# Kernel optimization log

Measured on AMD Instinct MI355X. Metric: run time of the kernel, lower is better.

Reference implementation:

```python
import jax, jax.numpy as jnp
import numpy as np

# dims
P = 512          # perception_vector_size
A_DIM = 64       # action_vector_size
D_MODEL = 256
D_STATE = 16
D_CONV = 4
D_INNER = 2 * D_MODEL      # expand=2 -> 512
DT_RANK = D_MODEL // 16    # ceil(256/16) = 16
BATCH = 8192


def setup_inputs() -> dict:
    key = jax.random.key(0)
    ks = jax.random.split(key, 12)
    s = lambda k, shp, sc=0.02: (jax.random.normal(k, shp, jnp.float32) * sc)
    return {
        "perception": jax.random.normal(ks[0], (BATCH, P), jnp.float32),
        # Brain linears
        "W_in": s(ks[1], (D_MODEL, P)), "b_in": jnp.zeros((D_MODEL,), jnp.float32),
        "mu_w": s(ks[2], (A_DIM, D_MODEL)), "mu_b": jnp.zeros((A_DIM,), jnp.float32),
        "ls_w": s(ks[3], (A_DIM, D_MODEL)), "ls_b": jnp.zeros((A_DIM,), jnp.float32),
        # Mamba params (mamba_ssm Mamba(d_model=256, d_state=16, d_conv=4, expand=2))
        "in_proj_w": s(ks[4], (2 * D_INNER, D_MODEL)),            # no bias
        "conv_w": s(ks[5], (D_INNER, D_CONV), 0.1),               # depthwise causal conv
        "conv_b": jnp.zeros((D_INNER,), jnp.float32),
        "x_proj_w": s(ks[6], (DT_RANK + 2 * D_STATE, D_INNER)),   # no bias
        "dt_proj_w": s(ks[7], (D_INNER, DT_RANK), 0.1),
        "dt_proj_b": s(ks[8], (D_INNER,), 0.1),
        # S4D real init: A_log[d, n] = log(n+1)
        "A_log": jnp.log(jnp.broadcast_to(jnp.arange(1, D_STATE + 1, dtype=jnp.float32), (D_INNER, D_STATE))),
        "Dskip": jnp.ones((D_INNER,), jnp.float32),
        "out_proj_w": s(ks[9], (D_MODEL, D_INNER)),               # no bias
    }


def _mamba(x, in_proj_w, conv_w, conv_b, x_proj_w, dt_proj_w, dt_proj_b, A_log, Dskip):
    # x: [B, L, d_model]
    Bsz, L, _ = x.shape
    xz = x @ in_proj_w.T                       # [B, L, 2*D_INNER]
    u, z = jnp.split(xz, 2, axis=-1)           # each [B, L, D_INNER]
    # causal depthwise conv1d (padding d_conv-1 on the left), then SiLU
    u_pad = jnp.pad(u, ((0, 0), (D_CONV - 1, 0), (0, 0)))
    idx = jnp.arange(L)[:, None] + jnp.arange(D_CONV)[None, :]   # [L, K]
    windows = u_pad[:, idx, :]                 # [B, L, K, D_INNER]
    u = jnp.einsum('blkc,ck->blc', windows, conv_w) + conv_b
    u = jax.nn.silu(u)
    # input-dependent SSM params
    x_dbl = u @ x_proj_w.T                     # [B, L, dt_rank + 2*d_state]
    dt, Bm, Cm = jnp.split(x_dbl, [DT_RANK, DT_RANK + D_STATE], axis=-1)
    delta = jax.nn.softplus(dt @ dt_proj_w.T + dt_proj_b)  # [B, L, D_INNER]
    A = -jnp.exp(A_log)                        # [D_INNER, D_STATE]

    def step(h, inp):
        u_t, dl, b_t, c_t = inp                # [B,D],[B,D],[B,N],[B,N]
        dA = jnp.exp(dl[..., None] * A)        # [B, D, N]
        h = dA * h + dl[..., None] * b_t[:, None, :] * u_t[..., None]
        y = jnp.einsum('bdn,bn->bd', h, c_t)
        return h, y

    h0 = jnp.zeros((Bsz, D_INNER, D_STATE), u.dtype)
    xs = (u.transpose(1, 0, 2), delta.transpose(1, 0, 2),
          Bm.transpose(1, 0, 2), Cm.transpose(1, 0, 2))
    _, ys = jax.lax.scan(step, h0, xs)         # ys: [L, B, D_INNER]
    y = ys.transpose(1, 0, 2) + Dskip * u      # skip connection D*u
    return y * jax.nn.silu(z)


def reference(perception, W_in, b_in, mu_w, mu_b, ls_w, ls_b,
              in_proj_w, conv_w, conv_b, x_proj_w, dt_proj_w, dt_proj_b,
              A_log, Dskip, out_proj_w):
    x = (perception @ W_in.T + b_in)[:, None, :]     # [B, 1, d_model]
    y = _mamba(x, in_proj_w, conv_w, conv_b, x_proj_w,
               dt_proj_w, dt_proj_b, A_log, Dskip)   # [B, 1, D_INNER]
    h = (y @ out_proj_w.T)[:, 0, :]                  # [B, d_model]
    mu = jnp.tanh(h @ mu_w.T + mu_b)
    log_std = jnp.clip(h @ ls_w.T + ls_b, -5.0, 2.0)
    return mu, log_std
```

## Files before the change

kernel.cpp:

```cpp
#include <hip/hip_runtime.h>
#include <hip/hip_fp16.h>
#include <cmath>

#define BATCH 8192

typedef short bf16x8 __attribute__((ext_vector_type(8)));
typedef float f32x4 __attribute__((ext_vector_type(4)));
typedef float f32x16 __attribute__((ext_vector_type(16)));

__device__ __forceinline__ void split2(float x, unsigned short& h, unsigned short& l){
    unsigned u = __float_as_uint(x);
    unsigned hr = u + 0x7fffu + ((u >> 16) & 1u);
    unsigned short hs = (unsigned short)(hr >> 16);
    float hf = __uint_as_float(((unsigned)hs) << 16);
    float d = x - hf;
    unsigned v = __float_as_uint(d);
    unsigned short ls = (unsigned short)((v + 0x7fffu + ((v >> 16) & 1u)) >> 16);
    h = hs; l = ls;
}
__device__ __forceinline__ float fsig(float x){ return 1.f / (1.f + __expf(-x)); }
__device__ __forceinline__ float ftanh(float x){
    x = fminf(fmaxf(x, -10.f), 10.f);
    const float e = __expf(2.f*x);
    return (e - 1.f) / (e + 1.f);
}
__device__ __forceinline__ void async_copy16(void* lds, const void* g){
    __builtin_amdgcn_global_load_lds(
        (const __attribute__((address_space(1))) unsigned int*)g,
        (__attribute__((address_space(3))) unsigned int*)lds, 16, 0, 0);
}


__global__ __launch_bounds__(256) void prep_all(
    const float* __restrict__ percep,
    const float* __restrict__ in_proj, const float* __restrict__ W_in,
    const float* __restrict__ b_in,
    const float* __restrict__ mu_w, const float* __restrict__ ls_w,
    const float* __restrict__ conv_w, const float* __restrict__ conv_b,
    const float* __restrict__ out_proj, const float* __restrict__ x_proj,
    unsigned short* __restrict__ W1h, unsigned short* __restrict__ W1l,
    unsigned short* __restrict__ Wth, unsigned short* __restrict__ Wtl,
    unsigned short* __restrict__ Xph, unsigned short* __restrict__ Xpl,
    unsigned short* __restrict__ Ph, unsigned short* __restrict__ Pl,
    float* __restrict__ b1)
{
    __shared__ float As[16][68];
    __shared__ float Ws[16][68];
    __shared__ unsigned short Lh[4096];
    __shared__ unsigned short Ll[4096];

    const int bx = blockIdx.x, by = blockIdx.y;
    const int tid = threadIdx.x;
    if (bx >= 20){
        const int s = (bx-20)*8 + by;
        const int band = s >> 4, ks = s & 15;
        const size_t tbase = (size_t)s*4096;
#pragma unroll
        for (int g=0; g<2; ++g){
            const int u = g*256 + tid;
            const int row = u >> 2, piece = u & 3;
            const float* src = percep + (size_t)(band*128 + row)*512 + ks*32 + piece*8;
            const float4 v0 = *reinterpret_cast<const float4*>(src);
            const float4 v1 = *reinterpret_cast<const float4*>(src+4);
            unsigned short h[8], l[8];
            split2(v0.x,h[0],l[0]); split2(v0.y,h[1],l[1]);
            split2(v0.z,h[2],l[2]); split2(v0.w,h[3],l[3]);
            split2(v1.x,h[4],l[4]); split2(v1.y,h[5],l[5]);
            split2(v1.z,h[6],l[6]); split2(v1.w,h[7],l[7]);
            uint4 H, L;
            H.x=(unsigned)h[0]|((unsigned)h[1]<<16); H.y=(unsigned)h[2]|((unsigned)h[3]<<16);
            H.z=(unsigned)h[4]|((unsigned)h[5]<<16); H.w=(unsigned)h[6]|((unsigned)h[7]<<16);
            L.x=(unsigned)l[0]|((unsigned)l[1]<<16); L.y=(unsigned)l[2]|((unsigned)l[3]<<16);
            L.z=(unsigned)l[4]|((unsigned)l[5]<<16); L.w=(unsigned)l[6]|((unsigned)l[7]<<16);
            const int off = piece*1024 + row*8;
            *reinterpret_cast<uint4*>(&Lh[off]) = H;
            *reinterpret_cast<uint4*>(&Ll[off]) = L;
        }
        __syncthreads();
#pragma unroll
        for (int g=0; g<2; ++g){
            const int f = g*256 + tid;
            *reinterpret_cast<uint4*>(&Ph[tbase + f*8]) = *reinterpret_cast<const uint4*>(&Lh[f*8]);
            *reinterpret_cast<uint4*>(&Pl[tbase + f*8]) = *reinterpret_cast<const uint4*>(&Ll[f*8]);
        }
        return;
    }
    if (bx == 18){
        const int lane = tid & 63, w = tid >> 6;
        const float4 bv = *reinterpret_cast<const float4*>(&b_in[lane*4]);
        const int nbase = by*128 + w*32;
#pragma unroll 4
        for (int i=0;i<32;i++){
            const int n = nbase + i;
            const float4 av = *reinterpret_cast<const float4*>(&in_proj[(size_t)n*256 + lane*4]);
            float p = av.x*bv.x + av.y*bv.y + av.z*bv.z + av.w*bv.w;
#pragma unroll
            for (int off=32; off; off>>=1) p += __shfl_xor(p, off, 64);
            if (lane == 0)
                b1[n] = (n < 512) ? fmaf(p, conv_w[n*4+3], conv_b[n]) : p;
        }
        return;
    }
    if (bx == 19){
        const int c0 = by*64;
#pragma unroll
        for (int p=0;p<16;p++){
            const int idx = p*256 + tid;
            const int rrow = idx >> 6;
            const int c = c0 + (idx & 63);
            const float v = (rrow < 48) ? x_proj[(size_t)rrow*512 + c] : 0.f;
            unsigned short h,l; split2(v,h,l);
            const int ks = c >> 5, r = (c >> 3) & 3, pos = c & 7;
            const size_t off = (size_t)ks*2048 + (r*64 + rrow)*8 + pos;
            Xph[off]=h; Xpl[off]=l;
        }
        return;
    }
    const float* A; unsigned short *Oh, *Ol; int m0; bool wt;
    const float* B;
    if (bx < 16){ A = in_proj + (size_t)bx*64*256; B = W_in; Oh=W1h; Ol=W1l; m0=bx*64; wt=false; }
    else { A = (bx==16 ? mu_w : ls_w); B = out_proj; Oh=Wth; Ol=Wtl; m0=(bx-16)*64; wt=true; }
    const int n0 = by*64;

    const int tm = tid/16, tn = tid%16;
    float acc[4][4];
#pragma unroll
    for (int i=0;i<4;i++)
#pragma unroll
      for (int j=0;j<4;j++) acc[i][j]=0.f;

    for (int k0=0;k0<256;k0+=16){
        {
            const int kf = tid & 3, mm = tid >> 2;
            float4 v = *reinterpret_cast<const float4*>(A + (size_t)mm*256 + k0 + kf*4);
            As[kf*4+0][mm]=v.x; As[kf*4+1][mm]=v.y; As[kf*4+2][mm]=v.z; As[kf*4+3][mm]=v.w;
        }
        {
            const int nn4 = tid & 15, kk = tid >> 4;
            float4 v = *reinterpret_cast<const float4*>(B + (size_t)(k0+kk)*512 + n0 + nn4*4);
            *reinterpret_cast<float4*>(&Ws[kk][nn4*4]) = v;
        }
        __syncthreads();
#pragma unroll
        for (int k=0;k<16;k++){
            const float4 av = *reinterpret_cast<const float4*>(&As[k][tm*4]);
            const float4 bv = *reinterpret_cast<const float4*>(&Ws[k][tn*4]);
            float a[4]={av.x,av.y,av.z,av.w}, b[4]={bv.x,bv.y,bv.z,bv.w};
#pragma unroll
            for (int i=0;i<4;i++)
#pragma unroll
                for (int j=0;j<4;j++) acc[i][j] = fmaf(a[i], b[j], acc[i][j]);
        }
        __syncthreads();
    }
#pragma unroll
    for (int i=0;i<4;i++){
        const int gm = m0 + tm*4 + i;
        const float s = (!wt && gm < 512) ? conv_w[gm*4+3] : 1.f;
        const int n = n0 + tn*4;
        unsigned short h[4], l[4];
#pragma unroll
        for (int j=0;j<4;j++) split2(acc[i][j]*s, h[j], l[j]);
        const int ks = n >> 5, r = (n >> 3) & 3, pos = n & 7;
        size_t off;
        if (wt) off = (size_t)ks*4096 + (r*128 + gm)*8 + pos;
        else    off = (size_t)((gm>>7)*16 + ks)*4096 + (r*128 + (gm&127))*8 + pos;
        *reinterpret_cast<ushort4*>(&Oh[off]) = make_ushort4(h[0],h[1],h[2],h[3]);
        *reinterpret_cast<ushort4*>(&Ol[off]) = make_ushort4(l[0],l[1],l[2],l[3]);
    }
}

__global__ __launch_bounds__(256,2) void mgemm6(
    const unsigned short* __restrict__ AhT, const unsigned short* __restrict__ AlT,
    const unsigned short* __restrict__ BhT, const unsigned short* __restrict__ BlT,
    const float* __restrict__ bias,
    float* __restrict__ O0, __half* __restrict__ O1)
{
    constexpr int TM=128, TN=128, WM=64, WN=64;
    constexpr int WAVES_N = TN/WN;
    constexpr int MT = WM/32, NT = WN/32;
    constexpr int PL = 4096;
    constexpr int NK = 16;

    const int tid = threadIdx.x;
    const int mb = blockIdx.x, nb = blockIdx.y;
    const int m0 = mb * TM, n0 = nb * TN;
    const int lane = tid & 63, wid = tid >> 6;
    const int half = lane >> 5, l32 = lane & 31;
    const int wm = (wid / WAVES_N) * WM;
    const int wn = (wid % WAVES_N) * WN;

    f32x16 acc[MT][NT];
#pragma unroll
    for (int i=0;i<MT;i++)
#pragma unroll
      for (int j=0;j<NT;j++)
#pragma unroll
        for (int r=0;r<16;r++) acc[i][j][r] = 0.f;

    const unsigned short* Ah0 = AhT + (size_t)mb*NK*PL;
    const unsigned short* Al0 = AlT + (size_t)mb*NK*PL;
    const unsigned short* Bh0 = BhT + (size_t)nb*NK*PL;
    const unsigned short* Bl0 = BlT + (size_t)nb*NK*PL;

#pragma unroll
    for (int k=0; k<NK; ++k){
        const unsigned short* ap = Ah0 + k*PL;
        const unsigned short* alp = Al0 + k*PL;
        const unsigned short* bp = Bh0 + k*PL;
        const unsigned short* blp = Bl0 + k*PL;

        bf16x8 ah[2][MT], al[2][MT], bh[2][NT], bl[2][NT];
#pragma unroll
        for (int j=0;j<2;j++){
            const int r = j*2 + half;
#pragma unroll
            for (int mt=0; mt<MT; ++mt){
                const int off = (r*TM + wm + mt*32 + l32)*8;
                ah[j][mt] = *reinterpret_cast<const bf16x8*>(&ap[off]);
                al[j][mt] = *reinterpret_cast<const bf16x8*>(&alp[off]);
            }
#pragma unroll
            for (int nt=0; nt<NT; ++nt){
                const int off = (r*TN + wn + nt*32 + l32)*8;
                bh[j][nt] = *reinterpret_cast<const bf16x8*>(&bp[off]);
                bl[j][nt] = *reinterpret_cast<const bf16x8*>(&blp[off]);
            }
        }
#pragma unroll
        for (int j=0;j<2;j++){
#pragma unroll
            for (int mt=0; mt<MT; ++mt)
#pragma unroll
            for (int nt=0; nt<NT; ++nt)
                acc[mt][nt] = __builtin_amdgcn_mfma_f32_32x32x16_bf16(ah[j][mt], bh[j][nt], acc[mt][nt], 0,0,0);
#pragma unroll
            for (int mt=0; mt<MT; ++mt)
#pragma unroll
            for (int nt=0; nt<NT; ++nt)
                acc[mt][nt] = __builtin_amdgcn_mfma_f32_32x32x16_bf16(al[j][mt], bh[j][nt], acc[mt][nt], 0,0,0);
#pragma unroll
            for (int mt=0; mt<MT; ++mt)
#pragma unroll
            for (int nt=0; nt<NT; ++nt)
                acc[mt][nt] = __builtin_amdgcn_mfma_f32_32x32x16_bf16(ah[j][mt], bl[j][nt], acc[mt][nt], 0,0,0);
        }
    }

#pragma unroll
    for (int mt=0; mt<MT; ++mt)
#pragma unroll
    for (int nt=0; nt<NT; ++nt)
#pragma unroll
    for (int r=0; r<16; ++r){
        const int row = m0 + wm + mt*32 + (r&3) + 8*(r>>2) + 4*half;
        const int col = n0 + wn + nt*32 + l32;
        float v = acc[mt][nt][r] + bias[col];
        if (col < 512) O0[(size_t)row*512 + col] = v * fsig(v);
        else           O1[(size_t)row*512 + (col-512)] = __float2half(v);
    }
}

__global__ __launch_bounds__(256,2) void tail_fused3(
    const float* __restrict__ Uf, const __half* __restrict__ Zh,
    const unsigned short* __restrict__ XphT, const unsigned short* __restrict__ XplT,
    const unsigned short* __restrict__ WthT, const unsigned short* __restrict__ WtlT,
    const float* __restrict__ dtw, const float* __restrict__ dtb,
    const float* __restrict__ dskip,
    const float* __restrict__ mu_b, const float* __restrict__ ls_b,
    float* __restrict__ mu_o, float* __restrict__ ls_o)
{
    constexpr int TM = 16;
    constexpr int ROWB = 136;
    __shared__ unsigned short sYh[2][16*ROWB];
    __shared__ unsigned short sYl[2][16*ROWB];
    __shared__ float sxd[TM][49];
    __shared__ float sBC[TM];

    const int tid = threadIdx.x;
    const int m0 = blockIdx.x * TM;
    const int lane = tid & 63, wid = tid >> 6;
    const int quad = lane >> 4, l16 = lane & 15;
    const int q = wid;

    float2 uvp[4][4]; __half2 zvp[4][4];
#pragma unroll
    for (int c=0;c<4;++c){
        const int d0 = c*128 + 2*lane;
#pragma unroll
        for (int rr=0; rr<4; ++rr){
            const size_t off = (size_t)(m0 + q*4 + rr)*512 + d0;
            uvp[c][rr] = *reinterpret_cast<const float2*>(&Uf[off]);
            zvp[c][rr] = *reinterpret_cast<const __half2*>(&Zh[off]);
        }
    }
    float2 dbp[4], dkp[4];
#pragma unroll
    for (int c=0;c<4;++c){
        const int d0 = c*128 + 2*lane;
        dbp[c] = *reinterpret_cast<const float2*>(&dtb[d0]);
        dkp[c] = *reinterpret_cast<const float2*>(&dskip[d0]);
    }

    f32x4 acc = (f32x4){0.f,0.f,0.f,0.f};
    const float* arow = Uf + (size_t)(m0 + l16)*512 + quad*8;
    const int bxp = (quad*64 + wid*16 + l16)*8;
#pragma unroll
    for (int k=0; k<16; ++k){
        const float4 a0 = *reinterpret_cast<const float4*>(arow + k*32);
        const float4 a1 = *reinterpret_cast<const float4*>(arow + k*32 + 4);
        const bf16x8 bh = *reinterpret_cast<const bf16x8*>(&XphT[(size_t)k*2048 + bxp]);
        const bf16x8 bl = *reinterpret_cast<const bf16x8*>(&XplT[(size_t)k*2048 + bxp]);
        bf16x8 ah, al;
        {
            const float a[8] = {a0.x,a0.y,a0.z,a0.w,a1.x,a1.y,a1.z,a1.w};
            unsigned short h[8], l[8];
#pragma unroll
            for (int j=0;j<8;j++) split2(a[j], h[j], l[j]);
#pragma unroll
            for (int j=0;j<8;j++){ ah[j] = (short)h[j]; al[j] = (short)l[j]; }
        }
        acc = __builtin_amdgcn_mfma_f32_16x16x32_bf16(ah, bh, acc, 0,0,0);
        acc = __builtin_amdgcn_mfma_f32_16x16x32_bf16(al, bh, acc, 0,0,0);
        acc = __builtin_amdgcn_mfma_f32_16x16x32_bf16(ah, bl, acc, 0,0,0);
    }

    {
        const int colp = wid*16 + l16;
        if (colp < 48){
#pragma unroll
            for (int r=0;r<4;++r) sxd[quad*4 + r][colp] = acc[r];
        }
    }
    __syncthreads();
    if (tid < TM){
        float bc = 0.f;
#pragma unroll
        for (int n=0;n<16;n++) bc = fmaf(sxd[tid][16+n], sxd[tid][32+n], bc);
        sBC[tid] = bc;
    }
    __syncthreads();

    f32x4 oacc[2];
    oacc[0] = (f32x4){0.f,0.f,0.f,0.f};
    oacc[1] = (f32x4){0.f,0.f,0.f,0.f};

    const unsigned ybase = (unsigned)(lane >> 2)*68 + (unsigned)(lane & 3);

#pragma unroll
    for (int c=0; c<4; ++c){
        const int d0 = c*128 + 2*lane, d1 = d0 + 1;
        float w0[16], w1[16];
#pragma unroll
        for (int j=0;j<4;j++){
            const float4 a = *reinterpret_cast<const float4*>(&dtw[d0*16 + j*4]);
            w0[j*4]=a.x; w0[j*4+1]=a.y; w0[j*4+2]=a.z; w0[j*4+3]=a.w;
            const float4 b = *reinterpret_cast<const float4*>(&dtw[d1*16 + j*4]);
            w1[j*4]=b.x; w1[j*4+1]=b.y; w1[j*4+2]=b.z; w1[j*4+3]=b.w;
        }
        const float db0 = dbp[c].x, db1 = dbp[c].y;
        const float dk0 = dkp[c].x, dk1 = dkp[c].y;

        unsigned short* yh = sYh[c&1];
        unsigned short* yl = sYl[c&1];
#pragma unroll
        for (int rr=0; rr<4; ++rr){
            const int r = q*4 + rr;
            float xr[16];
#pragma unroll
            for (int j=0;j<16;j++) xr[j] = sxd[r][j];
            const float bc = sBC[r];
            float t0 = db0, t1 = db1;
#pragma unroll
            for (int j=0;j<16;j++){ t0 = fmaf(xr[j], w0[j], t0); t1 = fmaf(xr[j], w1[j], t1); }
            const float dl0 = (t0 > 20.f) ? t0 : __logf(1.f + __expf(t0));
            const float dl1 = (t1 > 20.f) ? t1 : __logf(1.f + __expf(t1));
            const float2 uv = uvp[c][rr];
            const __half2 zv = zvp[c][rr];
            const float z0 = __low2float(zv), z1 = __high2float(zv);
            const float y0 = uv.x * fmaf(dl0, bc, dk0) * (z0 * fsig(z0));
            const float y1 = uv.y * fmaf(dl1, bc, dk1) * (z1 * fsig(z1));
            unsigned short h0,l0,h1,l1;
            split2(y0,h0,l0); split2(y1,h1,l1);
            reinterpret_cast<unsigned*>(yh)[ybase + r*4] = (unsigned)h0 | ((unsigned)h1<<16);
            reinterpret_cast<unsigned*>(yl)[ybase + r*4] = (unsigned)l0 | ((unsigned)l1<<16);
        }
        __syncthreads();

#pragma unroll
        for (int s=0; s<4; ++s){
            const int kt = c*4 + s;
            const int aoff = (4*s + quad)*ROWB + l16*8;
            const bf16x8 ya = *reinterpret_cast<const bf16x8*>(&yh[aoff]);
            const bf16x8 yl8 = *reinterpret_cast<const bf16x8*>(&yl[aoff]);
            bf16x8 bh2[2], bl2[2];
#pragma unroll
            for (int nt=0; nt<2; ++nt){
                const size_t boff = (size_t)kt*4096 + (quad*128 + wid*32 + nt*16 + l16)*8;
                bh2[nt] = *reinterpret_cast<const bf16x8*>(&WthT[boff]);
                bl2[nt] = *reinterpret_cast<const bf16x8*>(&WtlT[boff]);
            }
#pragma unroll
            for (int nt=0; nt<2; ++nt)
                oacc[nt] = __builtin_amdgcn_mfma_f32_16x16x32_bf16(ya, bh2[nt], oacc[nt], 0,0,0);
#pragma unroll
            for (int nt=0; nt<2; ++nt)
                oacc[nt] = __builtin_amdgcn_mfma_f32_16x16x32_bf16(yl8, bh2[nt], oacc[nt], 0,0,0);
#pragma unroll
            for (int nt=0; nt<2; ++nt)
                oacc[nt] = __builtin_amdgcn_mfma_f32_16x16x32_bf16(ya, bl2[nt], oacc[nt], 0,0,0);
        }
    }

#pragma unroll
    for (int nt=0; nt<2; ++nt)
#pragma unroll
    for (int r=0; r<4; ++r){
        const int row = m0 + quad*4 + r;
        const int col = wid*32 + nt*16 + l16;
        const float v = oacc[nt][r];
        if (col < 64) mu_o[(size_t)row*64 + col] = ftanh(v + mu_b[col]);
        else          ls_o[(size_t)row*64 + (col-64)] = fminf(fmaxf(v + ls_b[col-64], -5.f), 2.f);
    }
}

extern "C" void kernel_launch(void* const* d_in, const int* in_sizes, int n_in,
                              void* d_out, int out_size, void* d_ws, size_t ws_size,
                              hipStream_t stream) {
    (void)in_sizes; (void)n_in; (void)out_size; (void)ws_size;
    const float* percep  = (const float*)d_in[0];
    const float* W_in    = (const float*)d_in[1];
    const float* b_in    = (const float*)d_in[2];
    const float* mu_w    = (const float*)d_in[3];
    const float* mu_b    = (const float*)d_in[4];
    const float* ls_w    = (const float*)d_in[5];
    const float* ls_b    = (const float*)d_in[6];
    const float* in_proj = (const float*)d_in[7];
    const float* conv_w  = (const float*)d_in[8];
    const float* conv_b  = (const float*)d_in[9];
    const float* x_proj  = (const float*)d_in[10];
    const float* dt_w    = (const float*)d_in[11];
    const float* dt_b    = (const float*)d_in[12];
    const float* Dskip   = (const float*)d_in[14];
    const float* out_proj= (const float*)d_in[15];

    char* ws = (char*)d_ws;
    const size_t MB = 1u<<20;
    unsigned short* W1h = (unsigned short*)(ws);
    unsigned short* W1l = (unsigned short*)(ws + 1*MB);
    unsigned short* Wth = (unsigned short*)(ws + 2*MB);
    unsigned short* Wtl = (unsigned short*)(ws + 2*MB + 128*1024);
    unsigned short* Xph = (unsigned short*)(ws + 2*MB + 256*1024);
    unsigned short* Xpl = (unsigned short*)(ws + 2*MB + 320*1024);
    float*          b1  = (float*)         (ws + 2*MB + 384*1024);
    unsigned short* Ph  = (unsigned short*)(ws + 4*MB);
    unsigned short* Pl  = (unsigned short*)(ws + 12*MB);
    float*          Uf  = (float*)         (ws + 20*MB);
    __half*         Zh  = (__half*)        (ws + 36*MB);

    float* mu_o = (float*)d_out;
    float* ls_o = (float*)d_out + (size_t)BATCH*64;

    dim3 blk(256);
    prep_all<<<dim3(148,8), blk, 0, stream>>>(
        percep, in_proj, W_in, b_in, mu_w, ls_w, conv_w, conv_b, out_proj, x_proj,
        W1h, W1l, Wth, Wtl, Xph, Xpl, Ph, Pl, b1);
    mgemm6<<<dim3(64,8), blk, 0, stream>>>(
        Ph, Pl, W1h, W1l, b1, Uf, Zh);
    tail_fused3<<<dim3(BATCH/16), blk, 0, stream>>>(
        Uf, Zh, Xph, Xpl, Wth, Wtl, dt_w, dt_b, Dskip, mu_b, ls_b, mu_o, ls_o);
}
```

Baseline: 169.6 us.

## Shrink tiles in prep and main GEMM kernels to raise block count and occupancy

The weight-folding part of the prep kernel now uses 32x32 tiles with one output row per thread, so the grid grows from 148x8 to 102x16 blocks. The split-bf16 MFMA GEMM drops from 128x128 to 64x128 block tiles, with each wave covering a single 32-row M tile. Its launch bound is raised to 4 blocks per SM. The goal is more parallel blocks across the GPU's compute units and higher occupancy. The cost is less register-level reuse of the B operand and more global loads per FLOP.

Measured after the change: 164.7 us (median of 2 runs). 2.9% less time.

```diff
diff --git a/kernel.cpp b/kernel.cpp
--- a/kernel.cpp
+++ b/kernel.cpp
@@ -23,11 +23,6 @@
     x = fminf(fmaxf(x, -10.f), 10.f);
     const float e = __expf(2.f*x);
     return (e - 1.f) / (e + 1.f);
-}
-__device__ __forceinline__ void async_copy16(void* lds, const void* g){
-    __builtin_amdgcn_global_load_lds(
-        (const __attribute__((address_space(1))) unsigned int*)g,
-        (__attribute__((address_space(3))) unsigned int*)lds, 16, 0, 0);
 }
 
 
@@ -44,15 +39,16 @@
     unsigned short* __restrict__ Ph, unsigned short* __restrict__ Pl,
     float* __restrict__ b1)
 {
-    __shared__ float As[16][68];
-    __shared__ float Ws[16][68];
+    __shared__ float As[16][33];
+    __shared__ float Ws[16][36];
     __shared__ unsigned short Lh[4096];
     __shared__ unsigned short Ll[4096];
 
     const int bx = blockIdx.x, by = blockIdx.y;
     const int tid = threadIdx.x;
-    if (bx >= 20){
-        const int s = (bx-20)*8 + by;
+
+    if (bx >= 38){
+        const int s = (bx-38)*16 + by;
         const int band = s >> 4, ks = s & 15;
         const size_t tbase = (size_t)s*4096;
 #pragma unroll
@@ -85,12 +81,12 @@
         }
         return;
     }
-    if (bx == 18){
+    if (bx == 36){
         const int lane = tid & 63, w = tid >> 6;
         const float4 bv = *reinterpret_cast<const float4*>(&b_in[lane*4]);
-        const int nbase = by*128 + w*32;
+        const int nbase = by*64 + w*16;
 #pragma unroll 4
-        for (int i=0;i<32;i++){
+        for (int i=0;i<16;i++){
             const int n = nbase + i;
             const float4 av = *reinterpret_cast<const float4*>(&in_proj[(size_t)n*256 + lane*4]);
             float p = av.x*bv.x + av.y*bv.y + av.z*bv.z + av.w*bv.w;
@@ -101,13 +97,13 @@
         }
         return;
     }
-    if (bx == 19){
-        const int c0 = by*64;
-#pragma unroll
-        for (int p=0;p<16;p++){
+    if (bx == 37){
+        const int c0 = by*32;
+#pragma unroll
+        for (int p=0;p<8;p++){
             const int idx = p*256 + tid;
-            const int rrow = idx >> 6;
-            const int c = c0 + (idx & 63);
+            const int rrow = idx >> 5;
+            const int c = c0 + (idx & 31);
             const float v = (rrow < 48) ? x_proj[(size_t)rrow*512 + c] : 0.f;
             unsigned short h,l; split2(v,h,l);
             const int ks = c >> 5, r = (c >> 3) & 3, pos = c & 7;
@@ -118,49 +114,47 @@
     }
     const float* A; unsigned short *Oh, *Ol; int m0; bool wt;
     const float* B;
-    if (bx < 16){ A = in_proj + (size_t)bx*64*256; B = W_in; Oh=W1h; Ol=W1l; m0=bx*64; wt=false; }
-    else { A = (bx==16 ? mu_w : ls_w); B = out_proj; Oh=Wth; Ol=Wtl; m0=(bx-16)*64; wt=true; }
-    const int n0 = by*64;
-
-    const int tm = tid/16, tn = tid%16;
-    float acc[4][4];
-#pragma unroll
-    for (int i=0;i<4;i++)
-#pragma unroll
-      for (int j=0;j<4;j++) acc[i][j]=0.f;
+    if (bx < 32){ A = in_proj + (size_t)bx*32*256; B = W_in; Oh=W1h; Ol=W1l; m0=bx*32; wt=false; }
+    else {
+        const int t = bx - 32;
+        A = (t < 2) ? (mu_w + (size_t)t*32*256) : (ls_w + (size_t)(t-2)*32*256);
+        B = out_proj; Oh=Wth; Ol=Wtl; m0=t*32; wt=true;
+    }
+    const int n0 = by*32;
+
+    const int tm = tid >> 3, tn = tid & 7;
+    float acc[4] = {0.f,0.f,0.f,0.f};
 
     for (int k0=0;k0<256;k0+=16){
         {
-            const int kf = tid & 3, mm = tid >> 2;
-            float4 v = *reinterpret_cast<const float4*>(A + (size_t)mm*256 + k0 + kf*4);
-            As[kf*4+0][mm]=v.x; As[kf*4+1][mm]=v.y; As[kf*4+2][mm]=v.z; As[kf*4+3][mm]=v.w;
+            const int row = tid >> 3, kf = (tid & 7)*2;
+            const float2 v = *reinterpret_cast<const float2*>(A + (size_t)row*256 + k0 + kf);
+            As[kf][row] = v.x; As[kf+1][row] = v.y;
         }
         {
-            const int nn4 = tid & 15, kk = tid >> 4;
-            float4 v = *reinterpret_cast<const float4*>(B + (size_t)(k0+kk)*512 + n0 + nn4*4);
-            *reinterpret_cast<float4*>(&Ws[kk][nn4*4]) = v;
+            const int kk = tid >> 4, c = (tid & 15)*2;
+            const float2 v = *reinterpret_cast<const float2*>(B + (size_t)(k0+kk)*512 + n0 + c);
+            Ws[kk][c] = v.x; Ws[kk][c+1] = v.y;
         }
         __syncthreads();
 #pragma unroll
         for (int k=0;k<16;k++){
-            const float4 av = *reinterpret_cast<const float4*>(&As[k][tm*4]);
+            const float a = As[k][tm];
             const float4 bv = *reinterpret_cast<const float4*>(&Ws[k][tn*4]);
-            float a[4]={av.x,av.y,av.z,av.w}, b[4]={bv.x,bv.y,bv.z,bv.w};
-#pragma unroll
-            for (int i=0;i<4;i++)
-#pragma unroll
-                for (int j=0;j<4;j++) acc[i][j] = fmaf(a[i], b[j], acc[i][j]);
+            acc[0] = fmaf(a, bv.x, acc[0]);
+            acc[1] = fmaf(a, bv.y, acc[1]);
+            acc[2] = fmaf(a, bv.z, acc[2]);
+            acc[3] = fmaf(a, bv.w, acc[3]);
         }
         __syncthreads();
     }
-#pragma unroll
-    for (int i=0;i<4;i++){
-        const int gm = m0 + tm*4 + i;
+    {
+        const int gm = m0 + tm;
         const float s = (!wt && gm < 512) ? conv_w[gm*4+3] : 1.f;
         const int n = n0 + tn*4;
         unsigned short h[4], l[4];
 #pragma unroll
-        for (int j=0;j<4;j++) split2(acc[i][j]*s, h[j], l[j]);
+        for (int j=0;j<4;j++) split2(acc[j]*s, h[j], l[j]);
         const int ks = n >> 5, r = (n >> 3) & 3, pos = n & 7;
         size_t off;
         if (wt) off = (size_t)ks*4096 + (r*128 + gm)*8 + pos;
@@ -170,92 +164,73 @@
     }
 }
 
-__global__ __launch_bounds__(256,2) void mgemm6(
+__global__ __launch_bounds__(256,4) void mgemm6b(
     const unsigned short* __restrict__ AhT, const unsigned short* __restrict__ AlT,
     const unsigned short* __restrict__ BhT, const unsigned short* __restrict__ BlT,
     const float* __restrict__ bias,
     float* __restrict__ O0, __half* __restrict__ O1)
 {
-    constexpr int TM=128, TN=128, WM=64, WN=64;
-    constexpr int WAVES_N = TN/WN;
-    constexpr int MT = WM/32, NT = WN/32;
-    constexpr int PL = 4096;
+    constexpr int TN=128, WN=64;
+    constexpr int NT = 2;
     constexpr int NK = 16;
 
     const int tid = threadIdx.x;
     const int mb = blockIdx.x, nb = blockIdx.y;
-    const int m0 = mb * TM, n0 = nb * TN;
+    const int m0 = mb * 64, n0 = nb * TN;
     const int lane = tid & 63, wid = tid >> 6;
     const int half = lane >> 5, l32 = lane & 31;
-    const int wm = (wid / WAVES_N) * WM;
-    const int wn = (wid % WAVES_N) * WN;
-
-    f32x16 acc[MT][NT];
-#pragma unroll
-    for (int i=0;i<MT;i++)
-#pragma unroll
-      for (int j=0;j<NT;j++)
-#pragma unroll
-        for (int r=0;r<16;r++) acc[i][j][r] = 0.f;
-
-    const unsigned short* Ah0 = AhT + (size_t)mb*NK*PL;
-    const unsigned short* Al0 = AlT + (size_t)mb*NK*PL;
-    const unsigned short* Bh0 = BhT + (size_t)nb*NK*PL;
-    const unsigned short* Bl0 = BlT + (size_t)nb*NK*PL;
+    const int wm = (wid >> 1) * 32;
+    const int wn = (wid & 1) * WN;
+
+    f32x16 acc[NT];
+#pragma unroll
+    for (int j=0;j<NT;j++)
+#pragma unroll
+      for (int r=0;r<16;r++) acc[j][r] = 0.f;
+
+    const int gm = m0 + wm + l32;
+    const size_t Atile0 = (size_t)((gm>>7)*16)*4096;
+    const int Ain = (gm & 127)*8;
+    const unsigned short* Bh0 = BhT + (size_t)nb*NK*4096;
+    const unsigned short* Bl0 = BlT + (size_t)nb*NK*4096;
 
 #pragma unroll
     for (int k=0; k<NK; ++k){
-        const unsigned short* ap = Ah0 + k*PL;
-        const unsigned short* alp = Al0 + k*PL;
-        const unsigned short* bp = Bh0 + k*PL;
-        const unsigned short* blp = Bl0 + k*PL;
-
-        bf16x8 ah[2][MT], al[2][MT], bh[2][NT], bl[2][NT];
+        const size_t at = Atile0 + (size_t)k*4096 + Ain;
+        bf16x8 ah[2], al[2], bh[2][NT], bl[2][NT];
 #pragma unroll
         for (int j=0;j<2;j++){
             const int r = j*2 + half;
-#pragma unroll
-            for (int mt=0; mt<MT; ++mt){
-                const int off = (r*TM + wm + mt*32 + l32)*8;
-                ah[j][mt] = *reinterpret_cast<const bf16x8*>(&ap[off]);
-                al[j][mt] = *reinterpret_cast<const bf16x8*>(&alp[off]);
+            ah[j] = *reinterpret_cast<const bf16x8*>(&AhT[at + r*1024]);
+            al[j] = *reinterpret_cast<const bf16x8*>(&AlT[at + r*1024]);
+#pragma unroll
+            for (int nt=0; nt<NT; ++nt){
+                const size_t off = (size_t)k*4096 + (r*TN + wn + nt*32 + l32)*8;
+                bh[j][nt] = *reinterpret_cast<const bf16x8*>(&Bh0[off]);
+                bl[j][nt] = *reinterpret_cast<const bf16x8*>(&Bl0[off]);
             }
-#pragma unroll
-            for (int nt=0; nt<NT; ++nt){
-                const int off = (r*TN + wn + nt*32 + l32)*8;
-                bh[j][nt] = *reinterpret_cast<const bf16x8*>(&bp[off]);
-                bl[j][nt] = *reinterpret_cast<const bf16x8*>(&blp[off]);
-            }
         }
 #pragma unroll
         for (int j=0;j<2;j++){
 #pragma unroll
-            for (int mt=0; mt<MT; ++mt)
-#pragma unroll
             for (int nt=0; nt<NT; ++nt)
-                acc[mt][nt] = __builtin_amdgcn_mfma_f32_32x32x16_bf16(ah[j][mt], bh[j][nt], acc[mt][nt], 0,0,0);
-#pragma unroll
-            for (int mt=0; mt<MT; ++mt)
+                acc[nt] = __builtin_amdgcn_mfma_f32_32x32x16_bf16(ah[j], bh[j][nt], acc[nt], 0,0,0);
 #pragma unroll
             for (int nt=0; nt<NT; ++nt)
-                acc[mt][nt] = __builtin_amdgcn_mfma_f32_32x32x16_bf16(al[j][mt], bh[j][nt], acc[mt][nt], 0,0,0);
-#pragma unroll
-            for (int mt=0; mt<MT; ++mt)
+                acc[nt] = __builtin_amdgcn_mfma_f32_32x32x16_bf16(al[j], bh[j][nt], acc[nt], 0,0,0);
 #pragma unroll
             for (int nt=0; nt<NT; ++nt)
-                acc[mt][nt] = __builtin_amdgcn_mfma_f32_32x32x16_bf16(ah[j][mt], bl[j][nt], acc[mt][nt], 0,0,0);
-        }
-    }
-
-#pragma unroll
-    for (int mt=0; mt<MT; ++mt)
+                acc[nt] = __builtin_amdgcn_mfma_f32_32x32x16_bf16(ah[j], bl[j][nt], acc[nt], 0,0,0);
+        }
+    }
+
 #pragma unroll
     for (int nt=0; nt<NT; ++nt)
 #pragma unroll
     for (int r=0; r<16; ++r){
-        const int row = m0 + wm + mt*32 + (r&3) + 8*(r>>2) + 4*half;
+        const int row = m0 + wm + (r&3) + 8*(r>>2) + 4*half;
         const int col = n0 + wn + nt*32 + l32;
-        float v = acc[mt][nt][r] + bias[col];
+        float v = acc[nt][r] + bias[col];
         if (col < 512) O0[(size_t)row*512 + col] = v * fsig(v);
         else           O1[(size_t)row*512 + (col-512)] = __float2half(v);
     }
@@ -462,10 +437,10 @@
     float* ls_o = (float*)d_out + (size_t)BATCH*64;
 
     dim3 blk(256);
-    prep_all<<<dim3(148,8), blk, 0, stream>>>(
+    prep_all<<<dim3(102,16), blk, 0, stream>>>(
         percep, in_proj, W_in, b_in, mu_w, ls_w, conv_w, conv_b, out_proj, x_proj,
         W1h, W1l, Wth, Wtl, Xph, Xpl, Ph, Pl, b1);
-    mgemm6<<<dim3(64,8), blk, 0, stream>>>(
+    mgemm6b<<<dim3(128,8), blk, 0, stream>>>(
         Ph, Pl, W1h, W1l, b1, Uf, Zh);
     tail_fused3<<<dim3(BATCH/16), blk, 0, stream>>>(
         Uf, Zh, Xph, Xpl, Wth, Wtl, dt_w, dt_b, Dskip, mu_b, ls_b, mu_o, ls_o);
```
